# Kernel optimization log

Hardware: AMD Instinct MI355X
Metric: run time of the kernel (lower is better)

## Reference

```python
import jax, jax.numpy as jnp
import numpy as np

EPS = 1e-5
PATCH = 16


def silu(x):
    return x * jax.nn.sigmoid(x)


def rmsnorm(x, w):
    x = x.astype(jnp.float32)
    return x * jax.lax.rsqrt(jnp.mean(x * x, axis=-1, keepdims=True) + EPS) * w


def causal_conv1d(x, w, b):
    # x: [N, L, E]; w: [E, K] depthwise causal conv
    E, K = w.shape
    out = jax.lax.conv_general_dilated(
        jnp.swapaxes(x, 1, 2), w[:, None, :], (1,), [(K - 1, 0)],
        feature_group_count=E, dimension_numbers=('NCH', 'OIH', 'NCH'))
    return jnp.swapaxes(out + b[None, :, None], 1, 2)


def ssm_branch(xz, conv_w, conv_b, xproj, dtw, dtb, Alog, Dp):
    # One direction of a Mamba mixer: conv -> silu -> selective scan -> gate by silu(z)
    E, K = conv_w.shape
    S = Alog.shape[1]
    R = dtw.shape[1]
    u, z = xz[..., :E], xz[..., E:]
    u = silu(causal_conv1d(u, conv_w, conv_b))                      # [N,L,E]
    dbl = jnp.einsum('nle,re->nlr', u, xproj)                       # [N,L,R+2S]
    dt = jax.nn.softplus(jnp.einsum('nlr,er->nle', dbl[..., :R], dtw) + dtb)
    Bm, Cm = dbl[..., R:R + S], dbl[..., R + S:]
    A = -jnp.exp(Alog)                                              # [E,S]

    def step(h, inp):
        dt_t, u_t, B_t, C_t = inp                                   # [N,E],[N,E],[N,S],[N,S]
        h = jnp.exp(dt_t[..., None] * A) * h + (dt_t * u_t)[..., None] * B_t[:, None, :]
        return h, jnp.einsum('nes,ns->ne', h, C_t)

    h0 = jnp.zeros((u.shape[0], E, S), u.dtype)
    xs = (jnp.swapaxes(dt, 0, 1), jnp.swapaxes(u, 0, 1),
          jnp.swapaxes(Bm, 0, 1), jnp.swapaxes(Cm, 0, 1))
    _, ys = jax.lax.scan(step, h0, xs)
    y = jnp.swapaxes(ys, 0, 1) + u * Dp
    return y * silu(z)


def mamba(h, p, bimamba):
    xz = jnp.einsum('nld,ed->nle', h, p['inproj'])
    y = ssm_branch(xz, p['conv_w'], p['conv_b'], p['xproj'],
                   p['dtw'], p['dtb'], p['Alog'], p['D'])
    if bimamba:
        yr = ssm_branch(xz[:, ::-1], p['conv_w_r'], p['conv_b_r'], p['xproj_r'],
                        p['dtw_r'], p['dtb_r'], p['Alog_r'], p['D_r'])
        y = y + yr[:, ::-1]
    return jnp.einsum('nle,de->nld', y, p['outproj'])


def block(h, res, norm_w, p, bimamba):
    # fused add + RMSNorm (prenorm), residual kept in fp32
    res = h + res
    return mamba(rmsnorm(res, norm_w), p, bimamba), res


def setup_inputs() -> dict:
    key = jax.random.key(0)
    ks = iter(jax.random.split(key, 96))

    def rn(shape, scale=1.0):
        return jax.random.normal(next(ks), shape, jnp.float32) * scale

    D, E, S, R, K = 384, 768, 16, 24, 4
    NSP, NTM = 12, 12
    B, T = 2, 8
    Alog = jnp.log(jnp.tile(jnp.arange(1, S + 1, dtype=jnp.float32), (E, 1)))
    dtb0 = float(np.log(np.expm1(0.01)))  # inverse-softplus of dt_init=0.01
    inp = {
        'x': rn((B, 3, T, 224, 224)),
        'patch_w': rn((D, 3, 1, 16, 16), (3 * 16 * 16) ** -0.5),
        'patch_b': rn((D,), 0.02),
        'cls_token': rn((1, 1, D), 0.02),
        'pos_embed': rn((1, 197, D), 0.02),
        'normf': jnp.ones((D,), jnp.float32),
    }

    def add_branch(pref, suf, n):
        inp[pref + 'conv_w' + suf] = rn((n, E, K), K ** -0.5)
        inp[pref + 'conv_b' + suf] = jnp.zeros((n, E), jnp.float32)
        inp[pref + 'xproj' + suf] = rn((n, R + 2 * S, E), E ** -0.5)
        inp[pref + 'dtw' + suf] = rn((n, E, R), R ** -0.5)
        inp[pref + 'dtb' + suf] = jnp.full((n, E), dtb0, jnp.float32)
        inp[pref + 'Alog' + suf] = jnp.tile(Alog, (n, 1, 1))
        inp[pref + 'D' + suf] = jnp.ones((n, E), jnp.float32)

    add_branch('sp_', '', NSP)
    add_branch('sp_', '_r', NSP)
    add_branch('tm_', '', NTM)
    for pref, n in (('sp_', NSP), ('tm_', NTM)):
        inp[pref + 'norm'] = jnp.ones((n, D), jnp.float32)
        inp[pref + 'inproj'] = rn((n, 2 * E, D), D ** -0.5)
        inp[pref + 'outproj'] = rn((n, D, E), E ** -0.5)
    return inp


def reference(x, patch_w, patch_b, cls_token, pos_embed,
              sp_norm, sp_inproj, sp_outproj,
              sp_conv_w, sp_conv_b, sp_xproj, sp_dtw, sp_dtb, sp_Alog, sp_D,
              sp_conv_w_r, sp_conv_b_r, sp_xproj_r, sp_dtw_r, sp_dtb_r, sp_Alog_r, sp_D_r,
              tm_norm, tm_inproj, tm_outproj,
              tm_conv_w, tm_conv_b, tm_xproj, tm_dtw, tm_dtb, tm_Alog, tm_D,
              normf):
    B = x.shape[0]
    feat = jax.lax.conv_general_dilated(
        x, patch_w, (1, PATCH, PATCH), 'VALID',
        dimension_numbers=('NCDHW', 'OIDHW', 'NCDHW')) + patch_b[None, :, None, None, None]
    _, D, T, Hp, Wp = feat.shape
    Np = Hp * Wp
    tok = jnp.transpose(feat, (0, 2, 3, 4, 1)).reshape(B * T, Np, D)
    tok = jnp.concatenate([jnp.broadcast_to(cls_token, (B * T, 1, D)), tok], axis=1) + pos_embed
    P = Np + 1
    cls = tok[:, :1].reshape(B, T, 1, D)
    pt = tok[:, 1:].reshape(B, T, Np, D)
    # sinusoidal temporal position encoding over T
    pos = jnp.arange(T, dtype=jnp.float32)[:, None]
    div = 10000.0 ** (jnp.arange(0, D, 2, dtype=jnp.float32) / D)
    enc = jnp.stack([jnp.sin(pos / div), jnp.cos(pos / div)], axis=-1).reshape(T, D)
    pt = pt + enc[None, :, None, :]
    hidden = jnp.concatenate([cls, pt], axis=2)  # [B,T,P,D]
    residual = jnp.zeros_like(hidden)
    for i in range(sp_norm.shape[0]):  # bidirectional spatial blocks over (B*T, P, D)
        p = dict(inproj=sp_inproj[i], outproj=sp_outproj[i],
                 conv_w=sp_conv_w[i], conv_b=sp_conv_b[i], xproj=sp_xproj[i],
                 dtw=sp_dtw[i], dtb=sp_dtb[i], Alog=sp_Alog[i], D=sp_D[i],
                 conv_w_r=sp_conv_w_r[i], conv_b_r=sp_conv_b_r[i], xproj_r=sp_xproj_r[i],
                 dtw_r=sp_dtw_r[i], dtb_r=sp_dtb_r[i], Alog_r=sp_Alog_r[i], D_r=sp_D_r[i])
        h2, r2 = block(hidden.reshape(B * T, P, D), residual.reshape(B * T, P, D), sp_norm[i], p, True)
        hidden, residual = h2.reshape(B, T, P, D), r2.reshape(B, T, P, D)
    for i in range(tm_norm.shape[0]):  # unidirectional temporal blocks over (B, T*P, D)
        p = dict(inproj=tm_inproj[i], outproj=tm_outproj[i],
                 conv_w=tm_conv_w[i], conv_b=tm_conv_b[i], xproj=tm_xproj[i],
                 dtw=tm_dtw[i], dtb=tm_dtb[i], Alog=tm_Alog[i], D=tm_D[i])
        h2, r2 = block(hidden.reshape(B, T * P, D), residual.reshape(B, T * P, D), tm_norm[i], p, False)
        hidden, residual = h2.reshape(B, T, P, D), r2.reshape(B, T, P, D)
    return rmsnorm(hidden + residual, normf)
```

## Files before the change

### kernel.cpp

```cpp
#include <hip/hip_runtime.h>

#define NTOKS 3152
#define DMODEL 384
#define EDIM 768
#define TWOE 1536
#define SDIM 16
#define RDIM 24
#define XDIM 56
#define NLAYER 12
#define NPATCH 3136

typedef __attribute__((ext_vector_type(8))) short bf16x8;
typedef __attribute__((ext_vector_type(4))) float f32x4;

__device__ __forceinline__ float em_silu(float v) { return v / (1.f + __expf(-v)); }

__device__ __forceinline__ unsigned short f2bf(float f) {
  union { float f; unsigned int u; } v; v.f = f;
  const unsigned int r = v.u + 0x7fffu + ((v.u >> 16) & 1u);
  return (unsigned short)(r >> 16);
}
__device__ __forceinline__ unsigned int f2bf2(float lo, float hi) {
  return (unsigned int)f2bf(lo) | ((unsigned int)f2bf(hi) << 16);
}
__device__ __forceinline__ float bf2f(unsigned short s) {
  union { unsigned int u; float f; } v; v.u = (unsigned int)s << 16; return v.f;
}
__device__ __forceinline__ float bfbits_lo(unsigned int u) {
  union { unsigned int u; float f; } v; v.u = u << 16; return v.f;
}
__device__ __forceinline__ float bfbits_hi(unsigned int u) {
  union { unsigned int u; float f; } v; v.u = u & 0xffff0000u; return v.f;
}
__device__ __forceinline__ unsigned int addbf2(unsigned int a, unsigned int b) {
  return f2bf2(bfbits_lo(a) + bfbits_lo(b), bfbits_hi(a) + bfbits_hi(b));
}
__device__ __forceinline__ uint4 addbf8(uint4 a, uint4 b) {
  uint4 r;
  r.x = addbf2(a.x, b.x); r.y = addbf2(a.y, b.y);
  r.z = addbf2(a.z, b.z); r.w = addbf2(a.w, b.w);
  return r;
}
__device__ __forceinline__ float em_softplus(float a) {
  const float t = __expf(-fabsf(a));
  return fmaxf(a, 0.f) + __logf(1.f + t);
}

__device__ __forceinline__ void pow_chain16(float q, float* a) {
  const float q2 = q * q, q4 = q2 * q2, q8 = q4 * q4;
  a[0] = q;       a[1] = q2;      a[2] = q2 * q;  a[3] = q4;
  a[4] = q4 * q;  a[5] = q4 * q2; a[6] = q4 * a[2]; a[7] = q8;
  a[8] = q8 * q;  a[9] = q8 * q2; a[10] = q8 * a[2]; a[11] = q8 * q4;
  a[12] = q8 * a[4]; a[13] = q8 * a[5]; a[14] = q8 * a[6]; a[15] = q8 * q8;
}

__global__ __launch_bounds__(256)
void em_f2bf_arr(const float* __restrict__ s, unsigned short* __restrict__ d, size_t n) {
  const size_t i = ((size_t)blockIdx.x * 256 + threadIdx.x) * 4;
  if (i < n) {
    const float4 v = *reinterpret_cast<const float4*>(s + i);
    uint2 pk;
    pk.x = f2bf2(v.x, v.y); pk.y = f2bf2(v.z, v.w);
    *reinterpret_cast<uint2*>(d + i) = pk;
  }
}

__global__ __launch_bounds__(256)
void em_im2col(const float* __restrict__ x, unsigned short* __restrict__ col) {
  const int g = blockIdx.x * 256 + threadIdx.x;
  const int pr = g / 768;
  const int cc = g - pr * 768;
  const int np = pr % 196;
  const int bt = pr / 196;
  const int t = bt & 7, b = bt >> 3;
  const int hp = np / 14, wp = np - hp * 14;
  const int c = cc >> 8;
  const int rem = cc & 255;
  const int ph = rem >> 4, pw = rem & 15;
  col[g] = f2bf(x[(((size_t)(b * 3 + c) * 8 + t) * 224 + (hp * 16 + ph)) * 224 + (wp * 16 + pw)]);
}

__global__ __launch_bounds__(DMODEL)
void em_embed_norm(const float* __restrict__ tmpP, const float* __restrict__ pb,
                   const float* __restrict__ cls, const float* __restrict__ pos,
                   const float* __restrict__ w,
                   float* __restrict__ residual, unsigned short* __restrict__ xn_bf) {
  const int tok = blockIdx.x;
  const int d = threadIdx.x;
  const int p = tok % 197;
  const int bt = tok / 197;
  const int t = bt & 7;
  float v;
  if (p == 0) {
    v = cls[d] + pos[d];
  } else {
    const int np = p - 1;
    const float div = powf(10000.f, (float)(d & ~1) * (1.f / 384.f));
    const float ang = (float)t / div;
    const float enc = (d & 1) ? cosf(ang) : sinf(ang);
    v = tmpP[((size_t)bt * 196 + np) * DMODEL + d] + pb[d] + pos[(size_t)p * DMODEL + d] + enc;
  }
  const size_t idx = (size_t)tok * DMODEL + d;
  residual[idx] = v;
  float ss = v * v;
  #pragma unroll
  for (int off = 32; off; off >>= 1) ss += __shfl_xor(ss, off, 64);
  __shared__ float red[6];
  if ((d & 63) == 0) red[d >> 6] = ss;
  __syncthreads();
  float tot = 0.f;
  #pragma unroll
  for (int i = 0; i < 6; ++i) tot += red[i];
  const float scale = rsqrtf(tot * (1.f / 384.f) + 1e-5f);
  xn_bf[idx] = f2bf(v * scale * w[d]);
}

__global__ __launch_bounds__(DMODEL)
void em_add_rmsnorm(const float* __restrict__ hidden, const float* __restrict__ res_in,
                    float* __restrict__ res_out, const float* __restrict__ w,
                    float* __restrict__ out, unsigned short* __restrict__ out_bf) {
  const int tok = blockIdx.x;
  const int d = threadIdx.x;
  const size_t idx = (size_t)tok * DMODEL + d;
  const float v = hidden[idx] + res_in[idx];
  if (res_out) res_out[idx] = v;
  float ss = v * v;
  #pragma unroll
  for (int off = 32; off; off >>= 1) ss += __shfl_xor(ss, off, 64);
  __shared__ float red[6];
  if ((d & 63) == 0) red[d >> 6] = ss;
  __syncthreads();
  float tot = 0.f;
  #pragma unroll
  for (int i = 0; i < 6; ++i) tot += red[i];
  const float scale = rsqrtf(tot * (1.f / 384.f) + 1e-5f);
  const float r = v * scale * w[d];
  if (out_bf) out_bf[idx] = f2bf(r);
  else out[idx] = r;
}

#define TM 128
#define TN 64
#define LDT 40
__global__ __launch_bounds__(256)
void em_gemm_abf(const unsigned short* __restrict__ A, const unsigned short* __restrict__ A2,
                 const unsigned short* __restrict__ W, float* __restrict__ C,
                 int M, int N, int K) {
  __shared__ unsigned short As[TM * LDT];
  __shared__ unsigned short Bs[TN * LDT];
  const int tid = threadIdx.x;
  const int bm = blockIdx.y * TM;
  const int bn = blockIdx.x * TN;
  const int wave = tid >> 6, lane = tid & 63;
  const int wm = (wave >> 1) * 64, wn = (wave & 1) * 32;
  const int mq = lane & 15, quad = lane >> 4;
  f32x4 acc[4][2] = {};
  const int ar = tid >> 1;
  const int ah = (tid & 1) * 16;
  const int br = tid >> 2;
  const int bk = (tid & 3) * 8;

  for (int kk = 0; kk < K; kk += 32) {
    {
      uint4 v0 = {0, 0, 0, 0}, v1 = {0, 0, 0, 0};
      const int row = bm + ar;
      if (row < M) {
        const uint4* pa = reinterpret_cast<const uint4*>(A + (size_t)row * K + kk + ah);
        v0 = pa[0]; v1 = pa[1];
        if (A2) {
          const uint4* pb = reinterpret_cast<const uint4*>(A2 + (size_t)row * K + kk + ah);
          v0 = addbf8(v0, pb[0]); v1 = addbf8(v1, pb[1]);
        }
      }
      uint4* dst = reinterpret_cast<uint4*>(As + ar * LDT + ah);
      dst[0] = v0; dst[1] = v1;
    }
    *reinterpret_cast<uint4*>(Bs + br * LDT + bk) =
        *reinterpret_cast<const uint4*>(W + (size_t)(bn + br) * K + kk + bk);
    __syncthreads();
    bf16x8 bfr[2];
    #pragma unroll
    for (int j = 0; j < 2; ++j)
      bfr[j] = *reinterpret_cast<const bf16x8*>(Bs + (wn + j * 16 + mq) * LDT + quad * 8);
    #pragma unroll
    for (int i = 0; i < 4; ++i) {
      const bf16x8 afr = *reinterpret_cast<const bf16x8*>(As + (wm + i * 16 + mq) * LDT + quad * 8);
      acc[i][0] = __builtin_amdgcn_mfma_f32_16x16x32_bf16(afr, bfr[0], acc[i][0], 0, 0, 0);
      acc[i][1] = __builtin_amdgcn_mfma_f32_16x16x32_bf16(afr, bfr[1], acc[i][1], 0, 0, 0);
    }
    __syncthreads();
  }
  #pragma unroll
  for (int i = 0; i < 4; ++i) {
    const int mbase = bm + wm + i * 16 + quad * 4;
    #pragma unroll
    for (int j = 0; j < 2; ++j) {
      const int col = bn + wn + j * 16 + mq;
      #pragma unroll
      for (int p = 0; p < 4; ++p) {
        const int m = mbase + p;
        if (m < M) C[(size_t)m * N + col] = acc[i][j][p];
      }
    }
  }
}

__global__ __launch_bounds__(256)
void em_gemm_xpT(const unsigned short* __restrict__ ubf, const unsigned short* __restrict__ ubr,
                 const unsigned short* __restrict__ xpf, const unsigned short* __restrict__ xpr,
                 float* __restrict__ dblTf, float* __restrict__ dblTr) {
  const int dir = blockIdx.z;
  const int ks = blockIdx.y;
  const unsigned short* U = dir ? ubr : ubf;
  const unsigned short* W = dir ? xpr : xpf;
  float* C = dir ? dblTr : dblTf;
  __shared__ unsigned short As[64 * LDT];
  __shared__ unsigned short Bs[64 * LDT];
  const int tid = threadIdx.x;
  const int bn = blockIdx.x * 64;
  const int wave = tid >> 6, lane = tid & 63;
  const int wm = wave * 16;
  const int mq = lane & 15, quad = lane >> 4;
  f32x4 acc[4] = {};
  const int sr = tid >> 2;
  const int sq = (tid & 3) * 8;
  const int k0 = ks * (EDIM / 2), k1 = k0 + EDIM / 2;

  for (int kk = k0; kk < k1; kk += 32) {
    {
      uint4 pk = {0, 0, 0, 0};
      if (sr < XDIM)
        pk = *reinterpret_cast<const uint4*>(W + (size_t)sr * EDIM + kk + sq);
      *reinterpret_cast<uint4*>(As + sr * LDT + sq) = pk;
    }
    {
      uint4 v = {0, 0, 0, 0};
      const int tok = bn + sr;
      if (tok < NTOKS)
        v = *reinterpret_cast<const uint4*>(U + (size_t)tok * EDIM + kk + sq);
      *reinterpret_cast<uint4*>(Bs + sr * LDT + sq) = v;
    }
    __syncthreads();
    const bf16x8 afr = *reinterpret_cast<const bf16x8*>(As + (wm + mq) * LDT + quad * 8);
    #pragma unroll
    for (int j = 0; j < 4; ++j) {
      const bf16x8 bfr = *reinterpret_cast<const bf16x8*>(Bs + (j * 16 + mq) * LDT + quad * 8);
      acc[j] = __builtin_amdgcn_mfma_f32_16x16x32_bf16(afr, bfr, acc[j], 0, 0, 0);
    }
    __syncthreads();
  }
  #pragma unroll
  for (int j = 0; j < 4; ++j) {
    const int tok = bn + j * 16 + mq;
    if (tok < NTOKS) {
      #pragma unroll
      for (int p = 0; p < 4; ++p) {
        const int m = wm + quad * 4 + p;
        C[(size_t)(ks * 64 + m) * NTOKS + tok] = acc[j][p];
      }
    }
  }
}

#define DT_TT 16
__global__ __launch_bounds__(256)
void em_dtproj(const float* __restrict__ dblTf, const float* __restrict__ dblTr,
               const float* __restrict__ dtwf, const float* __restrict__ dtwr,
               const float* __restrict__ dtbf, const float* __restrict__ dtbr,
               float* __restrict__ dtf, float* __restrict__ dtr) {
  const int e = blockIdx.x * 256 + threadIdx.x;
  const int t0 = blockIdx.y * DT_TT;
  const int dir = blockIdx.z;
  const float* dblT = dir ? dblTr : dblTf;
  const float* dtw = dir ? dtwr : dtwf;
  const float* dtb = dir ? dtbr : dtbf;
  float* dto = dir ? dtr : dtf;
  __shared__ float r[DT_TT][RDIM + 1];
  for (int i = threadIdx.x; i < DT_TT * RDIM; i += 256) {
    const int tt = i & (DT_TT - 1);
    const int j = i >> 4;
    const int tok = t0 + tt;
    r[tt][j] = dblT[(size_t)j * NTOKS + tok] + dblT[(size_t)(64 + j) * NTOKS + tok];
  }
  __syncthreads();
  const float4* wp = reinterpret_cast<const float4*>(dtw + (size_t)e * RDIM);
  float w[RDIM];
  #pragma unroll
  for (int q = 0; q < 6; ++q) {
    const float4 v = wp[q];
    w[q * 4 + 0] = v.x; w[q * 4 + 1] = v.y; w[q * 4 + 2] = v.z; w[q * 4 + 3] = v.w;
  }
  const float b = dtb[e];
  float* o = dto + (size_t)t0 * EDIM + e;
  #pragma unroll 4
  for (int tt = 0; tt < DT_TT; ++tt) {
    float a = b;
    #pragma unroll
    for (int j = 0; j < RDIM; ++j) a += r[tt][j] * w[j];
    o[(size_t)tt * EDIM] = em_softplus(a);
  }
}

#define CONV_CT 16
__global__ __launch_bounds__(256)
void em_conv_silu(const float* __restrict__ xz,
                  const float* __restrict__ cwf, const float* __restrict__ cbf,
                  const float* __restrict__ cwr, const float* __restrict__ cbr,
                  unsigned short* __restrict__ ubf, unsigned short* __restrict__ ubr, int L) {
  const int e = blockIdx.x * 256 + threadIdx.x;
  const int t0 = blockIdx.y * CONV_CT;
  const int dir = blockIdx.z;
  const float* cw = dir ? cwr : cwf;
  const float* cb = dir ? cbr : cbf;
  unsigned short* out = dir ? ubr : ubf;
  const float4 wv = *reinterpret_cast<const float4*>(cw + e * 4);
  const float w0 = wv.x, w1 = wv.y, w2 = wv.z, w3 = wv.w;
  const float bv = cb[e];
  const float* xcol = xz + e;
  int l = t0 % L;
  if (dir == 0) {
    float xm1 = (l >= 1) ? xcol[(size_t)(t0 - 1) * TWOE] : 0.f;
    float xm2 = (l >= 2) ? xcol[(size_t)(t0 - 2) * TWOE] : 0.f;
    float xm3 = (l >= 3) ? xcol[(size_t)(t0 - 3) * TWOE] : 0.f;
    for (int tt = 0; tt < CONV_CT; ++tt) {
      const int tok = t0 + tt;
      if (tok >= NTOKS) break;
      const float xc = xcol[(size_t)tok * TWOE];
      float acc = bv + xc * w3;
      if (l >= 1) acc += xm1 * w2;
      if (l >= 2) acc += xm2 * w1;
      if (l >= 3) acc += xm3 * w0;
      out[(size_t)tok * EDIM + e] = f2bf(em_silu(acc));
      xm3 = xm2; xm2 = xm1; xm1 = xc;
      if (++l == L) l = 0;
    }
  } else {
    float xc  = xcol[(size_t)t0 * TWOE];
    float xp1 = (t0 + 1 < NTOKS) ? xcol[(size_t)(t0 + 1) * TWOE] : 0.f;
    float xp2 = (t0 + 2 < NTOKS) ? xcol[(size_t)(t0 + 2) * TWOE] : 0.f;
    for (int tt = 0; tt < CONV_CT; ++tt) {
      const int tok = t0 + tt;
      if (tok >= NTOKS) break;
      const float xp3 = (tok + 3 < NTOKS) ? xcol[(size_t)(tok + 3) * TWOE] : 0.f;
      float acc = bv + xc * w3;
      if (l + 1 < L) acc += xp1 * w2;
      if (l + 2 < L) acc += xp2 * w1;
      if (l + 3 < L) acc += xp3 * w0;
      out[(size_t)tok * EDIM + e] = f2bf(em_silu(acc));
      xc = xp1; xp1 = xp2; xp2 = xp3;
      if (++l == L) l = 0;
    }
  }
}

template<int CL, bool PW>
__device__ __forceinline__ void scan_sum_core(
    const float* __restrict__ dt, const unsigned short* __restrict__ u,
    const float (* __restrict__ Bs)[SDIM], const float* __restrict__ A,
    float* __restrict__ h, float* __restrict__ Pp, float& dsum,
    int n, int L, int p0, int len, int dir, int e) {
  auto step = [&](int j) {
    const int pos = p0 + j;
    const int l = dir ? (L - 1 - pos) : pos;
    const size_t tok = (size_t)n * L + l;
    const float dtv = dt[tok * EDIM + e];
    const float dtu = dtv * bf2f(u[tok * EDIM + e]);
    float a[SDIM];
    if (PW) {
      dsum += dtv;
      pow_chain16(__expf(-dtv), a);
    } else {
      #pragma unroll
      for (int s = 0; s < SDIM; ++s) a[s] = __expf(dtv * A[s]);
    }
    const float4* b4 = reinterpret_cast<const float4*>(Bs[j]);
    float bb[SDIM];
    #pragma unroll
    for (int q = 0; q < 4; ++q) {
      const float4 v = b4[q];
      bb[4*q] = v.x; bb[4*q+1] = v.y; bb[4*q+2] = v.z; bb[4*q+3] = v.w;
    }
    #pragma unroll
    for (int s = 0; s < SDIM; ++s) {
      h[s] = a[s] * h[s] + dtu * bb[s];
      if (!PW) Pp[s] *= a[s];
    }
  };
  if (len == CL) {
    #pragma unroll
    for (int j = 0; j < CL; ++j) step(j);
  } else {
    for (int j = 0; j < len; ++j) step(j);
  }
}

template<int CL>
__global__ __launch_bounds__(256)
void em_scan_sum(const float* __restrict__ dtf, const float* __restrict__ dtr,
                 const unsigned short* __restrict__ ubf, const unsigned short* __restrict__ ubr,
                 const float* __restrict__ dblTf, const float* __restrict__ dblTr,
                 const float* __restrict__ Alogf, const float* __restrict__ Alogr,
                 float* __restrict__ Pfw, float* __restrict__ Prv,
                 float* __restrict__ Hfw, float* __restrict__ Hrv,
                 int L, int nchunks) {
  const int dir = blockIdx.z;
  const int n = blockIdx.y / nchunks;
  const int c = blockIdx.y % nchunks;
  const int tid = threadIdx.x;
  const int e = blockIdx.x * 256 + tid;
  const float* dt = dir ? dtr : dtf;
  const unsigned short* u = dir ? ubr : ubf;
  const float* dblT = dir ? dblTr : dblTf;
  const float* Alog = dir ? Alogr : Alogf;
  float* P = dir ? Prv : Pfw;
  float* H = dir ? Hrv : Hfw;
  const int p0 = c * CL;
  const int len = min(CL, L - p0);
  __shared__ __align__(16) float Bs[CL][SDIM];
  for (int i = tid; i < CL * SDIM; i += 256) {
    const int j = i % CL, s = i / CL;
    if (j < len) {
      const int pos = p0 + j;
      const int l = dir ? (L - 1 - pos) : pos;
      const size_t col = (size_t)n * L + l;
      Bs[j][s] = dblT[(size_t)(RDIM + s) * NTOKS + col]
               + dblT[(size_t)(64 + RDIM + s) * NTOKS + col];
    }
  }
  __syncthreads();
  float A[SDIM], h[SDIM], Pp[SDIM];
  bool pw = true;
  #pragma unroll
  for (int s = 0; s < SDIM; ++s) {
    A[s] = -__expf(Alog[e * SDIM + s]);
    pw = pw && (fabsf(A[s] + (float)(s + 1)) < 1e-3f * (float)(s + 1));
    h[s] = 0.f;
  }
  float dsum = 0.f;
  if (pw) {
    scan_sum_core<CL, true>(dt, u, Bs, A, h, Pp, dsum, n, L, p0, len, dir, e);
    pow_chain16(__expf(-dsum), Pp);
  } else {
    #pragma unroll
    for (int s = 0; s < SDIM; ++s) Pp[s] = 1.f;
    scan_sum_core<CL, false>(dt, u, Bs, A, h, Pp, dsum, n, L, p0, len, dir, e);
  }
  const size_t base = ((size_t)(n * nchunks + c) * EDIM + e) * SDIM;
  #pragma unroll
  for (int s = 0; s < SDIM; ++s) { P[base + s] = Pp[s]; H[base + s] = h[s]; }
}

__global__ __launch_bounds__(256)
void em_scan_combine(const float* __restrict__ Pfw, const float* __restrict__ Prv,
                     float* __restrict__ Hfw, float* __restrict__ Hrv, int nchunks) {
  const int dir = blockIdx.z;
  const int idx = blockIdx.x * 256 + threadIdx.x;
  const int n = idx / (EDIM * SDIM);
  const int r = idx % (EDIM * SDIM);
  const float* P = dir ? Prv : Pfw;
  float* H = dir ? Hrv : Hfw;
  const size_t st = (size_t)EDIM * SDIM;
  size_t b = (size_t)n * nchunks * st + r;
  float h = 0.f;
  for (int c0 = 0; c0 < nchunks; c0 += 8) {
    float pv[8], hf[8];
    #pragma unroll
    for (int q = 0; q < 8; ++q)
      if (c0 + q < nchunks) { pv[q] = P[b + (size_t)q * st]; hf[q] = H[b + (size_t)q * st]; }
    #pragma unroll
    for (int q = 0; q < 8; ++q)
      if (c0 + q < nchunks) { H[b + (size_t)q * st] = h; h = pv[q] * h + hf[q]; }
    b += 8 * st;
  }
}

template<int CL, bool PW>
__device__ __forceinline__ void scan_out_core(
    const float* __restrict__ dt, const unsigned short* __restrict__ u,
    const float* __restrict__ xz, unsigned short* __restrict__ y,
    const float (* __restrict__ Bs)[SDIM], const float (* __restrict__ Cs)[SDIM],
    const float* __restrict__ A, float* __restrict__ h, float De,
    int n, int L, int p0, int len, int dir, int e) {
  auto step = [&](int j) {
    const int pos = p0 + j;
    const int l = dir ? (L - 1 - pos) : pos;
    const size_t tok = (size_t)n * L + l;
    const float dtv = dt[tok * EDIM + e];
    const float uv = bf2f(u[tok * EDIM + e]);
    const float dtu = dtv * uv;
    float a[SDIM];
    if (PW) {
      pow_chain16(__expf(-dtv), a);
    } else {
      #pragma unroll
      for (int s = 0; s < SDIM; ++s) a[s] = __expf(dtv * A[s]);
    }
    const float4* b4 = reinterpret_cast<const float4*>(Bs[j]);
    const float4* c4 = reinterpret_cast<const float4*>(Cs[j]);
    float bb[SDIM], cc[SDIM];
    #pragma unroll
    for (int q = 0; q < 4; ++q) {
      const float4 vb = b4[q], vc = c4[q];
      bb[4*q] = vb.x; bb[4*q+1] = vb.y; bb[4*q+2] = vb.z; bb[4*q+3] = vb.w;
      cc[4*q] = vc.x; cc[4*q+1] = vc.y; cc[4*q+2] = vc.z; cc[4*q+3] = vc.w;
    }
    float acc = 0.f;
    #pragma unroll
    for (int s = 0; s < SDIM; ++s) {
      h[s] = a[s] * h[s] + dtu * bb[s];
      acc += h[s] * cc[s];
    }
    const float z = xz[tok * TWOE + EDIM + e];
    y[tok * EDIM + e] = f2bf((acc + uv * De) * em_silu(z));
  };
  if (len == CL) {
    #pragma unroll
    for (int j = 0; j < CL; ++j) step(j);
  } else {
    for (int j = 0; j < len; ++j) step(j);
  }
}

template<int CL>
__global__ __launch_bounds__(256)
void em_scan_out(const float* __restrict__ dtf, const float* __restrict__ dtr,
                 const unsigned short* __restrict__ ubf, const unsigned short* __restrict__ ubr,
                 const float* __restrict__ dblTf, const float* __restrict__ dblTr,
                 const float* __restrict__ xz,
                 const float* __restrict__ Alogf, const float* __restrict__ Alogr,
                 const float* __restrict__ Dpf, const float* __restrict__ Dpr,
                 const float* __restrict__ Hfw, const float* __restrict__ Hrv,
                 unsigned short* __restrict__ ybf, unsigned short* __restrict__ ybr,
                 int L, int nchunks) {
  const int dir = blockIdx.z;
  const int n = blockIdx.y / nchunks;
  const int c = blockIdx.y % nchunks;
  const int tid = threadIdx.x;
  const int e = blockIdx.x * 256 + tid;
  const float* dt = dir ? dtr : dtf;
  const unsigned short* u = dir ? ubr : ubf;
  const float* dblT = dir ? dblTr : dblTf;
  const float* Alog = dir ? Alogr : Alogf;
  const float* Dp = dir ? Dpr : Dpf;
  const float* Hin = dir ? Hrv : Hfw;
  unsigned short* y = dir ? ybr : ybf;
  const int p0 = c * CL;
  const int len = min(CL, L - p0);
  __shared__ __align__(16) float Bs[CL][SDIM];
  __shared__ __align__(16) float Cs[CL][SDIM];
  for (int i = tid; i < CL * 2 * SDIM; i += 256) {
    const int j = i % CL, v = i / CL;
    if (j < len) {
      const int pos = p0 + j;
      const int l = dir ? (L - 1 - pos) : pos;
      const size_t col = (size_t)n * L + l;
      const float val = dblT[(size_t)(RDIM + v) * NTOKS + col]
                      + dblT[(size_t)(64 + RDIM + v) * NTOKS + col];
      if (v < SDIM) Bs[j][v] = val; else Cs[j][v - SDIM] = val;
    }
  }
  __syncthreads();
  float A[SDIM], h[SDIM];
  bool pw = true;
  const size_t base = ((size_t)(n * nchunks + c) * EDIM + e) * SDIM;
  #pragma unroll
  for (int s = 0; s < SDIM; ++s) {
    A[s] = -__expf(Alog[e * SDIM + s]);
    pw = pw && (fabsf(A[s] + (float)(s + 1)) < 1e-3f * (float)(s + 1));
    h[s] = Hin[base + s];
  }
  const float De = Dp[e];
  if (pw) scan_out_core<CL, true>(dt, u, xz, y, Bs, Cs, A, h, De, n, L, p0, len, dir, e);
  else    scan_out_core<CL, false>(dt, u, xz, y, Bs, Cs, A, h, De, n, L, p0, len, dir, e);
}

extern "C" void kernel_launch(void* const* d_in, const int* in_sizes, int n_in,
                              void* d_out, int out_size, void* d_ws, size_t ws_size,
                              hipStream_t stream) {
  const float* x         = (const float*)d_in[0];
  const float* patch_w   = (const float*)d_in[1];
  const float* patch_b   = (const float*)d_in[2];
  const float* cls_tok   = (const float*)d_in[3];
  const float* pos_emb   = (const float*)d_in[4];
  const float* normf     = (const float*)d_in[5];
  const float* sp_conv_w   = (const float*)d_in[6];
  const float* sp_conv_b   = (const float*)d_in[7];
  const float* sp_xproj    = (const float*)d_in[8];
  const float* sp_dtw      = (const float*)d_in[9];
  const float* sp_dtb      = (const float*)d_in[10];
  const float* sp_Alog     = (const float*)d_in[11];
  const float* sp_D        = (const float*)d_in[12];
  const float* sp_conv_w_r = (const float*)d_in[13];
  const float* sp_conv_b_r = (const float*)d_in[14];
  const float* sp_xproj_r  = (const float*)d_in[15];
  const float* sp_dtw_r    = (const float*)d_in[16];
  const float* sp_dtb_r    = (const float*)d_in[17];
  const float* sp_Alog_r   = (const float*)d_in[18];
  const float* sp_D_r      = (const float*)d_in[19];
  const float* tm_conv_w   = (const float*)d_in[20];
  const float* tm_conv_b   = (const float*)d_in[21];
  const float* tm_xproj    = (const float*)d_in[22];
  const float* tm_dtw      = (const float*)d_in[23];
  const float* tm_dtb      = (const float*)d_in[24];
  const float* tm_Alog     = (const float*)d_in[25];
  const float* tm_D        = (const float*)d_in[26];
  const float* sp_norm     = (const float*)d_in[27];
  const float* sp_inproj   = (const float*)d_in[28];
  const float* sp_outproj  = (const float*)d_in[29];
  const float* tm_norm     = (const float*)d_in[30];
  const float* tm_inproj   = (const float*)d_in[31];
  const float* tm_outproj  = (const float*)d_in[32];

  float* ws = (float*)d_ws;
  size_t o = 0;
  float* hidden   = ws + o; o += (size_t)NTOKS * DMODEL;
  float* residual = ws + o; o += (size_t)NTOKS * DMODEL;
  float* xz       = ws + o; o += (size_t)NTOKS * TWOE;
  float* dblT_f   = ws + o; o += (size_t)128 * NTOKS;
  float* dblT_r   = ws + o; o += (size_t)128 * NTOKS;
  float* dt_f     = ws + o; o += (size_t)NTOKS * EDIM;
  float* dt_r     = ws + o; o += (size_t)NTOKS * EDIM;
  unsigned short* xn_bf = (unsigned short*)(ws + o); o += (size_t)NTOKS * DMODEL / 2;
  unsigned short* ub_f  = (unsigned short*)(ws + o); o += (size_t)NTOKS * EDIM;
  unsigned short* ub_r  = ub_f + (size_t)NTOKS * EDIM;
  unsigned short* yb_f  = (unsigned short*)(ws + o); o += (size_t)NTOKS * EDIM;
  unsigned short* yb_r  = yb_f + (size_t)NTOKS * EDIM;

  const size_t n_inproj  = (size_t)NLAYER * TWOE * DMODEL;
  const size_t n_outproj = (size_t)NLAYER * DMODEL * EDIM;
  const size_t n_xproj   = (size_t)NLAYER * XDIM * EDIM;
  const size_t n_patch   = (size_t)DMODEL * 768;
  unsigned short* spin_bf  = (unsigned short*)(ws + o); o += n_inproj / 2;
  unsigned short* tmin_bf  = (unsigned short*)(ws + o); o += n_inproj / 2;
  unsigned short* spout_bf = (unsigned short*)(ws + o); o += n_outproj / 2;
  unsigned short* tmout_bf = (unsigned short*)(ws + o); o += n_outproj / 2;
  unsigned short* spxp_bf  = (unsigned short*)(ws + o); o += n_xproj / 2;
  unsigned short* spxpr_bf = (unsigned short*)(ws + o); o += n_xproj / 2;
  unsigned short* tmxp_bf  = (unsigned short*)(ws + o); o += n_xproj / 2;
  unsigned short* patch_bf = (unsigned short*)(ws + o); o += n_patch / 2;

  const size_t avail = (ws_size / sizeof(float) > o) ? (ws_size / sizeof(float) - o) : 0;
  int spCL = 16, tmCL = 8;
  size_t sets = 394;
  if (4 * sets * (size_t)(EDIM * SDIM) > avail) { tmCL = 16; sets = 208; }
  if (4 * sets * (size_t)(EDIM * SDIM) > avail) { spCL = 32; sets = 198; }
  const size_t sum_elems = sets * (size_t)EDIM * SDIM;
  float* scanP_f  = ws + o; o += sum_elems;
  float* scanP_r  = ws + o; o += sum_elems;
  float* scanH_f  = ws + o; o += sum_elems;
  float* scanH_r  = ws + o; o += sum_elems;

  unsigned short* im2col_bf = ub_f;
  float* patch_tmp = dt_f;

  const int L_sp = 197;
  const int L_tm = 1576;
  const int NC_sp = (L_sp + spCL - 1) / spCL;
  const int NC_tm = (L_tm + tmCL - 1) / tmCL;
  const int MT = (NTOKS + TM - 1) / TM;
  const int NT64 = (NTOKS + 63) / 64;
  const int NTC = (NTOKS + CONV_CT - 1) / CONV_CT;
  const int NT16 = NTOKS / DT_TT;

  auto cvt = [&](const float* s, unsigned short* d, size_t n) {
    em_f2bf_arr<<<(unsigned)((n / 4 + 255) / 256), 256, 0, stream>>>(s, d, n);
  };
  cvt(sp_inproj, spin_bf, n_inproj);
  cvt(tm_inproj, tmin_bf, n_inproj);
  cvt(sp_outproj, spout_bf, n_outproj);
  cvt(tm_outproj, tmout_bf, n_outproj);
  cvt(sp_xproj, spxp_bf, n_xproj);
  cvt(sp_xproj_r, spxpr_bf, n_xproj);
  cvt(tm_xproj, tmxp_bf, n_xproj);
  cvt(patch_w, patch_bf, n_patch);

  em_im2col<<<(NPATCH * 768) / 256, 256, 0, stream>>>(x, im2col_bf);
  em_gemm_abf<<<dim3(DMODEL / TN, (NPATCH + TM - 1) / TM), 256, 0, stream>>>(
      im2col_bf, nullptr, patch_bf, patch_tmp, NPATCH, DMODEL, 768);
  em_embed_norm<<<NTOKS, DMODEL, 0, stream>>>(patch_tmp, patch_b, cls_tok, pos_emb,
                                              sp_norm, residual, xn_bf);

  for (int i = 0; i < NLAYER; ++i) {
    em_gemm_abf<<<dim3(TWOE / TN, MT), 256, 0, stream>>>(
        xn_bf, nullptr, spin_bf + (size_t)i * TWOE * DMODEL, xz, NTOKS, TWOE, DMODEL);
    em_conv_silu<<<dim3(EDIM / 256, NTC, 2), 256, 0, stream>>>(
        xz, sp_conv_w + (size_t)i * EDIM * 4, sp_conv_b + (size_t)i * EDIM,
        sp_conv_w_r + (size_t)i * EDIM * 4, sp_conv_b_r + (size_t)i * EDIM,
        ub_f, ub_r, L_sp);
    em_gemm_xpT<<<dim3(NT64, 2, 2), 256, 0, stream>>>(
        ub_f, ub_r, spxp_bf + (size_t)i * XDIM * EDIM, spxpr_bf + (size_t)i * XDIM * EDIM,
        dblT_f, dblT_r);
    em_dtproj<<<dim3(EDIM / 256, NT16, 2), 256, 0, stream>>>(
        dblT_f, dblT_r, sp_dtw + (size_t)i * EDIM * RDIM, sp_dtw_r + (size_t)i * EDIM * RDIM,
        sp_dtb + (size_t)i * EDIM, sp_dtb_r + (size_t)i * EDIM, dt_f, dt_r);
    if (spCL == 16)
      em_scan_sum<16><<<dim3(EDIM / 256, 16 * NC_sp, 2), 256, 0, stream>>>(
          dt_f, dt_r, ub_f, ub_r, dblT_f, dblT_r,
          sp_Alog + (size_t)i * EDIM * SDIM, sp_Alog_r + (size_t)i * EDIM * SDIM,
          scanP_f, scanP_r, scanH_f, scanH_r, L_sp, NC_sp);
    else
      em_scan_sum<32><<<dim3(EDIM / 256, 16 * NC_sp, 2), 256, 0, stream>>>(
          dt_f, dt_r, ub_f, ub_r, dblT_f, dblT_r,
          sp_Alog + (size_t)i * EDIM * SDIM, sp_Alog_r + (size_t)i * EDIM * SDIM,
          scanP_f, scanP_r, scanH_f, scanH_r, L_sp, NC_sp);
    em_scan_combine<<<dim3(16 * EDIM * SDIM / 256, 1, 2), 256, 0, stream>>>(
        scanP_f, scanP_r, scanH_f, scanH_r, NC_sp);
    if (spCL == 16)
      em_scan_out<16><<<dim3(EDIM / 256, 16 * NC_sp, 2), 256, 0, stream>>>(
          dt_f, dt_r, ub_f, ub_r, dblT_f, dblT_r, xz,
          sp_Alog + (size_t)i * EDIM * SDIM, sp_Alog_r + (size_t)i * EDIM * SDIM,
          sp_D + (size_t)i * EDIM, sp_D_r + (size_t)i * EDIM,
          scanH_f, scanH_r, yb_f, yb_r, L_sp, NC_sp);
    else
      em_scan_out<32><<<dim3(EDIM / 256, 16 * NC_sp, 2), 256, 0, stream>>>(
          dt_f, dt_r, ub_f, ub_r, dblT_f, dblT_r, xz,
          sp_Alog + (size_t)i * EDIM * SDIM, sp_Alog_r + (size_t)i * EDIM * SDIM,
          sp_D + (size_t)i * EDIM, sp_D_r + (size_t)i * EDIM,
          scanH_f, scanH_r, yb_f, yb_r, L_sp, NC_sp);
    em_gemm_abf<<<dim3(DMODEL / TN, MT), 256, 0, stream>>>(
        yb_f, yb_r, spout_bf + (size_t)i * DMODEL * EDIM, hidden, NTOKS, DMODEL, EDIM);
    const float* next_w = (i < NLAYER - 1) ? sp_norm + (size_t)(i + 1) * DMODEL : tm_norm;
    em_add_rmsnorm<<<NTOKS, DMODEL, 0, stream>>>(hidden, residual, residual,
                                                 next_w, nullptr, xn_bf);
  }

  for (int i = 0; i < NLAYER; ++i) {
    em_gemm_abf<<<dim3(TWOE / TN, MT), 256, 0, stream>>>(
        xn_bf, nullptr, tmin_bf + (size_t)i * TWOE * DMODEL, xz, NTOKS, TWOE, DMODEL);
    em_conv_silu<<<dim3(EDIM / 256, NTC, 1), 256, 0, stream>>>(
        xz, tm_conv_w + (size_t)i * EDIM * 4, tm_conv_b + (size_t)i * EDIM,
        tm_conv_w + (size_t)i * EDIM * 4, tm_conv_b + (size_t)i * EDIM,
        ub_f, ub_r, L_tm);
    em_gemm_xpT<<<dim3(NT64, 2, 1), 256, 0, stream>>>(
        ub_f, ub_r, tmxp_bf + (size_t)i * XDIM * EDIM, tmxp_bf + (size_t)i * XDIM * EDIM,
        dblT_f, dblT_r);
    em_dtproj<<<dim3(EDIM / 256, NT16, 1), 256, 0, stream>>>(
        dblT_f, dblT_r, tm_dtw + (size_t)i * EDIM * RDIM, tm_dtw + (size_t)i * EDIM * RDIM,
        tm_dtb + (size_t)i * EDIM, tm_dtb + (size_t)i * EDIM, dt_f, dt_r);
    if (tmCL == 8)
      em_scan_sum<8><<<dim3(EDIM / 256, 2 * NC_tm, 1), 256, 0, stream>>>(
          dt_f, dt_r, ub_f, ub_r, dblT_f, dblT_r,
          tm_Alog + (size_t)i * EDIM * SDIM, tm_Alog + (size_t)i * EDIM * SDIM,
          scanP_f, scanP_r, scanH_f, scanH_r, L_tm, NC_tm);
    else
      em_scan_sum<16><<<dim3(EDIM / 256, 2 * NC_tm, 1), 256, 0, stream>>>(
          dt_f, dt_r, ub_f, ub_r, dblT_f, dblT_r,
          tm_Alog + (size_t)i * EDIM * SDIM, tm_Alog + (size_t)i * EDIM * SDIM,
          scanP_f, scanP_r, scanH_f, scanH_r, L_tm, NC_tm);
    em_scan_combine<<<dim3(2 * EDIM * SDIM / 256, 1, 1), 256, 0, stream>>>(
        scanP_f, scanP_r, scanH_f, scanH_r, NC_tm);
    if (tmCL == 8)
      em_scan_out<8><<<dim3(EDIM / 256, 2 * NC_tm, 1), 256, 0, stream>>>(
          dt_f, dt_r, ub_f, ub_r, dblT_f, dblT_r, xz,
          tm_Alog + (size_t)i * EDIM * SDIM, tm_Alog + (size_t)i * EDIM * SDIM,
          tm_D + (size_t)i * EDIM, tm_D + (size_t)i * EDIM,
          scanH_f, scanH_r, yb_f, yb_r, L_tm, NC_tm);
    else
      em_scan_out<16><<<dim3(EDIM / 256, 2 * NC_tm, 1), 256, 0, stream>>>(
          dt_f, dt_r, ub_f, ub_r, dblT_f, dblT_r, xz,
          tm_Alog + (size_t)i * EDIM * SDIM, tm_Alog + (size_t)i * EDIM * SDIM,
          tm_D + (size_t)i * EDIM, tm_D + (size_t)i * EDIM,
          scanH_f, scanH_r, yb_f, yb_r, L_tm, NC_tm);
    em_gemm_abf<<<dim3(DMODEL / TN, MT), 256, 0, stream>>>(
        yb_f, nullptr, tmout_bf + (size_t)i * DMODEL * EDIM, hidden, NTOKS, DMODEL, EDIM);
    const bool last = (i == NLAYER - 1);
    const float* next_w = last ? normf : tm_norm + (size_t)(i + 1) * DMODEL;
    em_add_rmsnorm<<<NTOKS, DMODEL, 0, stream>>>(hidden, residual, last ? nullptr : residual,
                                                 next_w, last ? (float*)d_out : nullptr,
                                                 last ? nullptr : xn_bf);
  }
}
```

Before: 3.333 ms.

## Double-buffer GEMM LDS tiles and split-K out-projection with fused partial sum

Both bf16 MFMA GEMM kernels now use two LDS buffers, so the global loads for the next K tile are issued before the current tile's MFMAs and only one barrier per iteration is needed. The out-projection GEMM (K=768, N=384) is additionally split into two K halves via blockIdx.z, writing two fp32 partial outputs that the following add+RMSNorm kernel sums. This doubles the block count of a small-N GEMM to fill more CUs and hides load latency, at the cost of doubled LDS use, extra fp32 partial-output traffic and one more read in the norm kernel.

```diff
diff --git a/kernel.cpp b/kernel.cpp
--- a/kernel.cpp
+++ b/kernel.cpp
@@ -116,13 +116,15 @@
 }
 
 __global__ __launch_bounds__(DMODEL)
-void em_add_rmsnorm(const float* __restrict__ hidden, const float* __restrict__ res_in,
+void em_add_rmsnorm(const float* __restrict__ hidden, const float* __restrict__ hidden2,
+                    const float* __restrict__ res_in,
                     float* __restrict__ res_out, const float* __restrict__ w,
                     float* __restrict__ out, unsigned short* __restrict__ out_bf) {
   const int tok = blockIdx.x;
   const int d = threadIdx.x;
   const size_t idx = (size_t)tok * DMODEL + d;
-  const float v = hidden[idx] + res_in[idx];
+  float v = hidden[idx] + res_in[idx];
+  if (hidden2) v += hidden2[idx];
   if (res_out) res_out[idx] = v;
   float ss = v * v;
   #pragma unroll
@@ -145,12 +147,14 @@
 __global__ __launch_bounds__(256)
 void em_gemm_abf(const unsigned short* __restrict__ A, const unsigned short* __restrict__ A2,
                  const unsigned short* __restrict__ W, float* __restrict__ C,
-                 int M, int N, int K) {
-  __shared__ unsigned short As[TM * LDT];
-  __shared__ unsigned short Bs[TN * LDT];
+                 int M, int N, int K, int KS) {
+  __shared__ unsigned short As[2][TM * LDT];
+  __shared__ unsigned short Bs[2][TN * LDT];
   const int tid = threadIdx.x;
   const int bm = blockIdx.y * TM;
   const int bn = blockIdx.x * TN;
+  const int kk0 = blockIdx.z * K;
+  const int kkend = kk0 + K;
   const int wave = tid >> 6, lane = tid & 63;
   const int wm = (wave >> 1) * 64, wn = (wave & 1) * 32;
   const int mq = lane & 15, quad = lane >> 4;
@@ -159,37 +163,51 @@
   const int ah = (tid & 1) * 16;
   const int br = tid >> 2;
   const int bk = (tid & 3) * 8;
-
-  for (int kk = 0; kk < K; kk += 32) {
-    {
-      uint4 v0 = {0, 0, 0, 0}, v1 = {0, 0, 0, 0};
-      const int row = bm + ar;
-      if (row < M) {
-        const uint4* pa = reinterpret_cast<const uint4*>(A + (size_t)row * K + kk + ah);
-        v0 = pa[0]; v1 = pa[1];
-        if (A2) {
-          const uint4* pb = reinterpret_cast<const uint4*>(A2 + (size_t)row * K + kk + ah);
-          v0 = addbf8(v0, pb[0]); v1 = addbf8(v1, pb[1]);
-        }
+  const int arow = bm + ar;
+
+  uint4 a0, a1, b0;
+  auto load_tile = [&](int kk) {
+    a0 = {0, 0, 0, 0}; a1 = {0, 0, 0, 0};
+    if (arow < M) {
+      const uint4* pa = reinterpret_cast<const uint4*>(A + (size_t)arow * KS + kk + ah);
+      a0 = pa[0]; a1 = pa[1];
+      if (A2) {
+        const uint4* pb = reinterpret_cast<const uint4*>(A2 + (size_t)arow * KS + kk + ah);
+        a0 = addbf8(a0, pb[0]); a1 = addbf8(a1, pb[1]);
       }
-      uint4* dst = reinterpret_cast<uint4*>(As + ar * LDT + ah);
-      dst[0] = v0; dst[1] = v1;
-    }
-    *reinterpret_cast<uint4*>(Bs + br * LDT + bk) =
-        *reinterpret_cast<const uint4*>(W + (size_t)(bn + br) * K + kk + bk);
-    __syncthreads();
+    }
+    b0 = *reinterpret_cast<const uint4*>(W + (size_t)(bn + br) * KS + kk + bk);
+  };
+  auto store_tile = [&](int buf) {
+    uint4* dst = reinterpret_cast<uint4*>(&As[buf][ar * LDT + ah]);
+    dst[0] = a0; dst[1] = a1;
+    *reinterpret_cast<uint4*>(&Bs[buf][br * LDT + bk]) = b0;
+  };
+
+  load_tile(kk0);
+  store_tile(0);
+  __syncthreads();
+  int cur = 0;
+  for (int kk = kk0; kk < kkend; kk += 32) {
+    const bool have = (kk + 32) < kkend;
+    if (have) load_tile(kk + 32);
     bf16x8 bfr[2];
     #pragma unroll
     for (int j = 0; j < 2; ++j)
-      bfr[j] = *reinterpret_cast<const bf16x8*>(Bs + (wn + j * 16 + mq) * LDT + quad * 8);
+      bfr[j] = *reinterpret_cast<const bf16x8*>(&Bs[cur][(wn + j * 16 + mq) * LDT + quad * 8]);
     #pragma unroll
     for (int i = 0; i < 4; ++i) {
-      const bf16x8 afr = *reinterpret_cast<const bf16x8*>(As + (wm + i * 16 + mq) * LDT + quad * 8);
+      const bf16x8 afr = *reinterpret_cast<const bf16x8*>(&As[cur][(wm + i * 16 + mq) * LDT + quad * 8]);
       acc[i][0] = __builtin_amdgcn_mfma_f32_16x16x32_bf16(afr, bfr[0], acc[i][0], 0, 0, 0);
       acc[i][1] = __builtin_amdgcn_mfma_f32_16x16x32_bf16(afr, bfr[1], acc[i][1], 0, 0, 0);
     }
-    __syncthreads();
-  }
+    if (have) {
+      store_tile(cur ^ 1);
+      __syncthreads();
+      cur ^= 1;
+    }
+  }
+  float* Cz = C + (size_t)blockIdx.z * M * N;
   #pragma unroll
   for (int i = 0; i < 4; ++i) {
     const int mbase = bm + wm + i * 16 + quad * 4;
@@ -199,7 +217,7 @@
       #pragma unroll
       for (int p = 0; p < 4; ++p) {
         const int m = mbase + p;
-        if (m < M) C[(size_t)m * N + col] = acc[i][j][p];
+        if (m < M) Cz[(size_t)m * N + col] = acc[i][j][p];
       }
     }
   }
@@ -214,8 +232,8 @@
   const unsigned short* U = dir ? ubr : ubf;
   const unsigned short* W = dir ? xpr : xpf;
   float* C = dir ? dblTr : dblTf;
-  __shared__ unsigned short As[64 * LDT];
-  __shared__ unsigned short Bs[64 * LDT];
+  __shared__ unsigned short As[2][64 * LDT];
+  __shared__ unsigned short Bs[2][64 * LDT];
   const int tid = threadIdx.x;
   const int bn = blockIdx.x * 64;
   const int wave = tid >> 6, lane = tid & 63;
@@ -225,29 +243,39 @@
   const int sr = tid >> 2;
   const int sq = (tid & 3) * 8;
   const int k0 = ks * (EDIM / 2), k1 = k0 + EDIM / 2;
-
+  const int btok = bn + sr;
+
+  uint4 wa, ub;
+  auto load_tile = [&](int kk) {
+    wa = {0, 0, 0, 0}; ub = {0, 0, 0, 0};
+    if (sr < XDIM)
+      wa = *reinterpret_cast<const uint4*>(W + (size_t)sr * EDIM + kk + sq);
+    if (btok < NTOKS)
+      ub = *reinterpret_cast<const uint4*>(U + (size_t)btok * EDIM + kk + sq);
+  };
+  auto store_tile = [&](int buf) {
+    *reinterpret_cast<uint4*>(&As[buf][sr * LDT + sq]) = wa;
+    *reinterpret_cast<uint4*>(&Bs[buf][sr * LDT + sq]) = ub;
+  };
+
+  load_tile(k0);
+  store_tile(0);
+  __syncthreads();
+  int cur = 0;
   for (int kk = k0; kk < k1; kk += 32) {
-    {
-      uint4 pk = {0, 0, 0, 0};
-      if (sr < XDIM)
-        pk = *reinterpret_cast<const uint4*>(W + (size_t)sr * EDIM + kk + sq);
-      *reinterpret_cast<uint4*>(As + sr * LDT + sq) = pk;
-    }
-    {
-      uint4 v = {0, 0, 0, 0};
-      const int tok = bn + sr;
-      if (tok < NTOKS)
-        v = *reinterpret_cast<const uint4*>(U + (size_t)tok * EDIM + kk + sq);
-      *reinterpret_cast<uint4*>(Bs + sr * LDT + sq) = v;
-    }
-    __syncthreads();
-    const bf16x8 afr = *reinterpret_cast<const bf16x8*>(As + (wm + mq) * LDT + quad * 8);
+    const bool have = (kk + 32) < k1;
+    if (have) load_tile(kk + 32);
+    const bf16x8 afr = *reinterpret_cast<const bf16x8*>(&As[cur][(wm + mq) * LDT + quad * 8]);
     #pragma unroll
     for (int j = 0; j < 4; ++j) {
-      const bf16x8 bfr = *reinterpret_cast<const bf16x8*>(Bs + (j * 16 + mq) * LDT + quad * 8);
+      const bf16x8 bfr = *reinterpret_cast<const bf16x8*>(&Bs[cur][(j * 16 + mq) * LDT + quad * 8]);
       acc[j] = __builtin_amdgcn_mfma_f32_16x16x32_bf16(afr, bfr, acc[j], 0, 0, 0);
     }
-    __syncthreads();
+    if (have) {
+      store_tile(cur ^ 1);
+      __syncthreads();
+      cur ^= 1;
+    }
   }
   #pragma unroll
   for (int j = 0; j < 4; ++j) {
@@ -613,7 +641,8 @@
 
   float* ws = (float*)d_ws;
   size_t o = 0;
-  float* hidden   = ws + o; o += (size_t)NTOKS * DMODEL;
+  float* hidden   = ws + o; o += (size_t)2 * NTOKS * DMODEL;
+  float* hidden2  = hidden + (size_t)NTOKS * DMODEL;
   float* residual = ws + o; o += (size_t)NTOKS * DMODEL;
   float* xz       = ws + o; o += (size_t)NTOKS * TWOE;
   float* dblT_f   = ws + o; o += (size_t)128 * NTOKS;
@@ -675,14 +704,14 @@
   cvt(patch_w, patch_bf, n_patch);
 
   em_im2col<<<(NPATCH * 768) / 256, 256, 0, stream>>>(x, im2col_bf);
-  em_gemm_abf<<<dim3(DMODEL / TN, (NPATCH + TM - 1) / TM), 256, 0, stream>>>(
-      im2col_bf, nullptr, patch_bf, patch_tmp, NPATCH, DMODEL, 768);
+  em_gemm_abf<<<dim3(DMODEL / TN, (NPATCH + TM - 1) / TM, 1), 256, 0, stream>>>(
+      im2col_bf, nullptr, patch_bf, patch_tmp, NPATCH, DMODEL, 768, 768);
   em_embed_norm<<<NTOKS, DMODEL, 0, stream>>>(patch_tmp, patch_b, cls_tok, pos_emb,
                                               sp_norm, residual, xn_bf);
 
   for (int i = 0; i < NLAYER; ++i) {
-    em_gemm_abf<<<dim3(TWOE / TN, MT), 256, 0, stream>>>(
-        xn_bf, nullptr, spin_bf + (size_t)i * TWOE * DMODEL, xz, NTOKS, TWOE, DMODEL);
+    em_gemm_abf<<<dim3(TWOE / TN, MT, 1), 256, 0, stream>>>(
+        xn_bf, nullptr, spin_bf + (size_t)i * TWOE * DMODEL, xz, NTOKS, TWOE, DMODEL, DMODEL);
     em_conv_silu<<<dim3(EDIM / 256, NTC, 2), 256, 0, stream>>>(
         xz, sp_conv_w + (size_t)i * EDIM * 4, sp_conv_b + (size_t)i * EDIM,
         sp_conv_w_r + (size_t)i * EDIM * 4, sp_conv_b_r + (size_t)i * EDIM,
@@ -717,16 +746,16 @@
           sp_Alog + (size_t)i * EDIM * SDIM, sp_Alog_r + (size_t)i * EDIM * SDIM,
           sp_D + (size_t)i * EDIM, sp_D_r + (size_t)i * EDIM,
           scanH_f, scanH_r, yb_f, yb_r, L_sp, NC_sp);
-    em_gemm_abf<<<dim3(DMODEL / TN, MT), 256, 0, stream>>>(
-        yb_f, yb_r, spout_bf + (size_t)i * DMODEL * EDIM, hidden, NTOKS, DMODEL, EDIM);
+    em_gemm_abf<<<dim3(DMODEL / TN, MT, 2), 256, 0, stream>>>(
+        yb_f, yb_r, spout_bf + (size_t)i * DMODEL * EDIM, hidden, NTOKS, DMODEL, EDIM / 2, EDIM);
     const float* next_w = (i < NLAYER - 1) ? sp_norm + (size_t)(i + 1) * DMODEL : tm_norm;
-    em_add_rmsnorm<<<NTOKS, DMODEL, 0, stream>>>(hidden, residual, residual,
+    em_add_rmsnorm<<<NTOKS, DMODEL, 0, stream>>>(hidden, hidden2, residual, residual,
                                                  next_w, nullptr, xn_bf);
   }
 
   for (int i = 0; i < NLAYER; ++i) {
-    em_gemm_abf<<<dim3(TWOE / TN, MT), 256, 0, stream>>>(
-        xn_bf, nullptr, tmin_bf + (size_t)i * TWOE * DMODEL, xz, NTOKS, TWOE, DMODEL);
+    em_gemm_abf<<<dim3(TWOE / TN, MT, 1), 256, 0, stream>>>(
+        xn_bf, nullptr, tmin_bf + (size_t)i * TWOE * DMODEL, xz, NTOKS, TWOE, DMODEL, DMODEL);
     em_conv_silu<<<dim3(EDIM / 256, NTC, 1), 256, 0, stream>>>(
         xz, tm_conv_w + (size_t)i * EDIM * 4, tm_conv_b + (size_t)i * EDIM,
         tm_conv_w + (size_t)i * EDIM * 4, tm_conv_b + (size_t)i * EDIM,
@@ -761,11 +790,12 @@
           tm_Alog + (size_t)i * EDIM * SDIM, tm_Alog + (size_t)i * EDIM * SDIM,
           tm_D + (size_t)i * EDIM, tm_D + (size_t)i * EDIM,
           scanH_f, scanH_r, yb_f, yb_r, L_tm, NC_tm);
-    em_gemm_abf<<<dim3(DMODEL / TN, MT), 256, 0, stream>>>(
-        yb_f, nullptr, tmout_bf + (size_t)i * DMODEL * EDIM, hidden, NTOKS, DMODEL, EDIM);
+    em_gemm_abf<<<dim3(DMODEL / TN, MT, 2), 256, 0, stream>>>(
+        yb_f, nullptr, tmout_bf + (size_t)i * DMODEL * EDIM, hidden, NTOKS, DMODEL, EDIM / 2, EDIM);
     const bool last = (i == NLAYER - 1);
     const float* next_w = last ? normf : tm_norm + (size_t)(i + 1) * DMODEL;
-    em_add_rmsnorm<<<NTOKS, DMODEL, 0, stream>>>(hidden, residual, last ? nullptr : residual,
+    em_add_rmsnorm<<<NTOKS, DMODEL, 0, stream>>>(hidden, hidden2, residual,
+                                                 last ? nullptr : residual,
                                                  next_w, last ? (float*)d_out : nullptr,
                                                  last ? nullptr : xn_bf);
   }
```

Result: faster. 3.218 ms (-3.4%).
